# Optimization experiments

Hardware: AMD Instinct MI355X
Metric: run time of the kernel (lower is better)

Reference implementation:

```python
import jax, jax.numpy as jnp
import numpy as np

V, F, P = 1024, 2048, 8192
_EPS = 1e-12


def setup_inputs() -> dict:
    key = jax.random.key(0)
    kv, kf, kp = jax.random.split(key, 3)
    verts = jax.random.normal(kv, (V, 3), dtype=jnp.float32)
    faces = jax.random.randint(kf, (F, 3), 0, V, dtype=jnp.int32)
    points = jax.random.normal(kp, (P, 3), dtype=jnp.float32)
    return {"verts": verts, "faces": faces, "points": points}


def _closest_point_on_tri(p, a, b, c):
    """Ericson's closest-point-on-triangle, broadcast over leading dims.
    p, a, b, c: [..., 3] -> closest point [..., 3]."""
    ab = b - a
    ac = c - a
    ap = p - a
    d1 = jnp.sum(ab * ap, -1)
    d2 = jnp.sum(ac * ap, -1)
    bp = p - b
    d3 = jnp.sum(ab * bp, -1)
    d4 = jnp.sum(ac * bp, -1)
    cp = p - c
    d5 = jnp.sum(ab * cp, -1)
    d6 = jnp.sum(ac * cp, -1)
    vc = d1 * d4 - d3 * d2
    vb = d5 * d2 - d1 * d6
    va = d3 * d6 - d5 * d4
    # guarded edge/interior parameters (denominators are >0 whenever the
    # corresponding region condition holds; eps keeps unselected branches finite)
    t_ab = d1 / jnp.maximum(d1 - d3, _EPS)
    t_ac = d2 / jnp.maximum(d2 - d6, _EPS)
    t_bc = (d4 - d3) / jnp.maximum((d4 - d3) + (d5 - d6), _EPS)
    denom = jnp.maximum(va + vb + vc, _EPS)
    v_in = vb / denom
    w_in = vc / denom
    # first-match region selection (vertex A, vertex B, edge AB, vertex C, edge AC, edge BC, interior)
    cA = (d1 <= 0) & (d2 <= 0)
    cB = (d3 >= 0) & (d4 <= d3)
    cAB = (vc <= 0) & (d1 >= 0) & (d3 <= 0)
    cC = (d6 >= 0) & (d5 <= d6)
    cAC = (vb <= 0) & (d2 >= 0) & (d6 <= 0)
    cBC = (va <= 0) & ((d4 - d3) >= 0) & ((d5 - d6) >= 0)
    z = jnp.zeros_like(d1)
    o = jnp.ones_like(d1)
    bv = jnp.select([cA, cB, cAB, cC, cAC, cBC], [z, o, t_ab, z, z, 1.0 - t_bc], v_in)
    bw = jnp.select([cA, cB, cAB, cC, cAC, cBC], [z, z, z, o, t_ac, t_bc], w_in)
    bu = 1.0 - bv - bw
    return a * bu[..., None] + b * bv[..., None] + c * bw[..., None]


def reference(verts, faces, points):
    tri = verts[faces]  # [F, 3, 3]
    a = tri[:, 0][None]  # [1, F, 3]
    b = tri[:, 1][None]
    c = tri[:, 2][None]
    cp = _closest_point_on_tri(points[:, None, :], a, b, c)  # [P, F, 3]
    dist2 = jnp.sum((points[:, None, :] - cp) ** 2, -1)  # [P, F] squared distances
    assoc = jnp.argmin(dist2, axis=1).astype(jnp.int32)  # [P] nearest triangle index
    dist = jnp.min(dist2, axis=1)  # [P]
    # loss_type == 'mse': kernel loss = sum(dist), then *= 1000 / P
    loss = jnp.sum(dist) * (1000.0 / points.shape[0])
    return loss, dist, assoc
```

## Files before the change

kernel.cpp:

```cpp
#include <hip/hip_runtime.h>
#include <float.h>

#define P_TOTAL 8192
#define F_TOTAL 2048
#define TPB     256
#define CHUNK   256
#define NCHUNK  (F_TOTAL / CHUNK)

__device__ __forceinline__ float refine_rcp(float D) {
#pragma clang fp contract(off)
    float r0 = __builtin_amdgcn_rcpf(D);
    float e1 = __builtin_fmaf(-D, r0, 1.0f);
    return __builtin_fmaf(e1, r0, r0);
}
__device__ __forceinline__ float div_rn(float num, float D, float r) {
#pragma clang fp contract(off)
    float q0 = num * r;
    float e  = __builtin_fmaf(-D, q0, num);
    return __builtin_fmaf(e, r, q0);
}

__device__ __forceinline__ void region_select(
    float d1, float d2, float d3, float d4, float d5, float d6,
    float va, float vb, float vc, float d43, float d56,
    float g1, float g2, float g3, float g4,
    float& bu, float& bv, float& bw)
{
#pragma clang fp contract(off)
    float G1 = fmaxf(g1, 1e-12f);
    float G2 = fmaxf(g2, 1e-12f);
    float G3 = fmaxf(g3, 1e-12f);
    float G4 = fmaxf(g4, 1e-12f);

    bool cA  = (d1 <= 0.f) & (d2 <= 0.f);
    bool cB  = (d3 >= 0.f) & (d4 <= d3);
    bool cAB = (vc <= 0.f) & (d1 >= 0.f) & (d3 <= 0.f);
    bool cC  = (d6 >= 0.f) & (d5 <= d6);
    bool cAC = (vb <= 0.f) & (d2 >= 0.f) & (d6 <= 0.f);
    bool cBC = (va <= 0.f) & (d43 >= 0.f) & (d56 >= 0.f);

    float nv = cA ? 0.f : cB ? 1.f : cAB ? d1 : cC ? 0.f
             : cAC ? 0.f : cBC ? d43 : vb;
    float nw = cA ? 0.f : cB ? 0.f : cAB ? 0.f : cC ? 1.f
             : cAC ? d2 : cBC ? d43 : vc;
    float D  = cA ? 1.f : cB ? 1.f : cAB ? G1 : cC ? 1.f
             : cAC ? G2 : cBC ? G3 : G4;
    bool fBC = cBC && !(cA || cB || cAB || cC || cAC);

    float r   = refine_rcp(D);
    float qv  = div_rn(nv, D, r);
    float bww = div_rn(nw, D, r);
    float bvv = fBC ? (1.0f - qv) : qv;
    bv = bvv; bw = bww;
    bu = (1.0f - bvv) - bww;
}

__device__ __forceinline__ float eval_exact(
    float px, float py, float pz,
    float ax, float ay, float az,
    float bx, float by, float bz,
    float cx, float cy, float cz)
{
#pragma clang fp contract(off)
    float abx = bx - ax, aby = by - ay, abz = bz - az;
    float acx = cx - ax, acy = cy - ay, acz = cz - az;
    float apx = px - ax, apy = py - ay, apz = pz - az;
    float d1 = (abx * apx + aby * apy) + abz * apz;
    float d2 = (acx * apx + acy * apy) + acz * apz;
    float bpx = px - bx, bpy = py - by, bpz = pz - bz;
    float d3 = (abx * bpx + aby * bpy) + abz * bpz;
    float d4 = (acx * bpx + acy * bpy) + acz * bpz;
    float cpx = px - cx, cpy = py - cy, cpz = pz - cz;
    float d5 = (abx * cpx + aby * cpy) + abz * cpz;
    float d6 = (acx * cpx + acy * cpy) + acz * cpz;

    float vc = d1 * d4 - d3 * d2;
    float vb = d5 * d2 - d1 * d6;
    float va = d3 * d6 - d5 * d4;
    float d43 = d4 - d3, d56 = d5 - d6;
    float g1 = d1 - d3, g2 = d2 - d6, g3 = d43 + d56, g4 = (va + vb) + vc;

    float bu, bv, bw;
    region_select(d1, d2, d3, d4, d5, d6, va, vb, vc, d43, d56,
                  g1, g2, g3, g4, bu, bv, bw);

    float cpx2 = (ax * bu + bx * bv) + cx * bw;
    float cpy2 = (ay * bu + by * bv) + cy * bw;
    float cpz2 = (az * bu + bz * bv) + cz * bw;
    float dx = px - cpx2, dy = py - cpy2, dz = pz - cpz2;
    return (dx * dx + dy * dy) + dz * dz;
}

__global__ __launch_bounds__(TPB) void msdf_main(
    const float* __restrict__ verts, const int* __restrict__ faces,
    const float* __restrict__ points, float* __restrict__ out)
{
    __shared__ float sT[13][CHUNK];
    __shared__ int   slist[4][CHUNK];
    const int tid  = threadIdx.x;
    const int lane = tid & 63;
    const int w    = tid >> 6;
    const int p    = blockIdx.x * 4 + w;

    const float px = points[3 * p], py = points[3 * p + 1], pz = points[3 * p + 2];

    unsigned int best_bits = 0xFFFFFFFFu;
    int best_idx = 0;
    float ub = FLT_MAX;

    for (int c = 0; c < NCHUNK; ++c) {
        __syncthreads();
        {
            int tg = c * CHUNK + tid;
            int i0 = faces[3 * tg + 0], i1 = faces[3 * tg + 1], i2 = faces[3 * tg + 2];
            float ax = verts[3 * i0], ay = verts[3 * i0 + 1], az = verts[3 * i0 + 2];
            float bx = verts[3 * i1], by = verts[3 * i1 + 1], bz = verts[3 * i1 + 2];
            float cx = verts[3 * i2], cy = verts[3 * i2 + 1], cz = verts[3 * i2 + 2];
            sT[0][tid] = ax; sT[1][tid] = ay; sT[2][tid] = az;
            sT[3][tid] = bx; sT[4][tid] = by; sT[5][tid] = bz;
            sT[6][tid] = cx; sT[7][tid] = cy; sT[8][tid] = cz;
            float e1x = bx - ax, e1y = by - ay, e1z = bz - az;
            float e2x = cx - ax, e2y = cy - ay, e2z = cz - az;
            float nx = e1y * e2z - e1z * e2y;
            float ny = e1z * e2x - e1x * e2z;
            float nz = e1x * e2y - e1y * e2x;
            float nn = (nx * nx + ny * ny) + nz * nz;
            float inv = (nn > 1e-30f) ? (1.0f / sqrtf(nn)) : 0.0f;
            nx *= inv; ny *= inv; nz *= inv;
            sT[9][tid] = nx; sT[10][tid] = ny; sT[11][tid] = nz;
            sT[12][tid] = (nx * ax + ny * ay) + nz * az;
        }
        __syncthreads();

        if (c == 0) {
            float u = FLT_MAX;
            #pragma unroll
            for (int s = 0; s < 4; ++s) {
                int t = s * 64 + lane;
                float dx = px - sT[0][t], dy = py - sT[1][t], dz = pz - sT[2][t];
                u = fminf(u, (dx * dx + dy * dy) + dz * dz);
            }
            #pragma unroll
            for (int off = 32; off; off >>= 1)
                u = fminf(u, __shfl_xor(u, off, 64));
            ub = fminf(ub, u);
        }

        int cnt = 0;
        const float ubm = ub * 1.02f + 1e-18f;
        #pragma unroll
        for (int s = 0; s < 4; ++s) {
            int t = s * 64 + lane;
            float lv = ((sT[9][t] * px + sT[10][t] * py) + sT[11][t] * pz) - sT[12][t];
            float lb = lv * lv;
            bool pred = (lb <= ubm);
            unsigned long long m = __ballot(pred);
            if (pred) {
                int off = (int)__popcll(m & ((1ull << lane) - 1ull));
                slist[w][cnt + off] = t;
            }
            cnt += (int)__popcll(m);
        }
        __threadfence_block();

        float ubc = FLT_MAX;
        for (int j = lane; j < cnt; j += 64) {
            int t = slist[w][j];
            float d2v = eval_exact(px, py, pz,
                sT[0][t], sT[1][t], sT[2][t],
                sT[3][t], sT[4][t], sT[5][t],
                sT[6][t], sT[7][t], sT[8][t]);
            unsigned int bits = __float_as_uint(d2v);
            int gi = c * CHUNK + t;
            if (bits < best_bits) { best_bits = bits; best_idx = gi; }
            ubc = fminf(ubc, d2v);
        }
        #pragma unroll
        for (int off = 32; off; off >>= 1)
            ubc = fminf(ubc, __shfl_xor(ubc, off, 64));
        ub = fminf(ub, ubc);
    }

    unsigned long long key =
        ((unsigned long long)best_bits << 32) | (unsigned int)best_idx;
    #pragma unroll
    for (int off = 32; off > 0; off >>= 1) {
        unsigned int hi = (unsigned int)(key >> 32);
        unsigned int lo = (unsigned int)(key & 0xFFFFFFFFu);
        unsigned int ohi = __shfl_down(hi, off, 64);
        unsigned int olo = __shfl_down(lo, off, 64);
        unsigned long long ok = ((unsigned long long)ohi << 32) | olo;
        key = (ok < key) ? ok : key;
    }
    if (lane == 0) {
        out[1 + p]           = __uint_as_float((unsigned int)(key >> 32));
        out[1 + P_TOTAL + p] = (float)(unsigned int)(key & 0xFFFFFFFFu);
    }
}

__global__ __launch_bounds__(256) void msdf_loss(float* __restrict__ out)
{
    __shared__ float wsum[4];
    float s = 0.f;
    for (int k = 0; k < P_TOTAL / 256; ++k)
        s += out[1 + k * 256 + threadIdx.x];
    #pragma unroll
    for (int off = 32; off > 0; off >>= 1) s += __shfl_down(s, off, 64);
    int lane = threadIdx.x & 63, w = threadIdx.x >> 6;
    if (lane == 0) wsum[w] = s;
    __syncthreads();
    if (threadIdx.x == 0) {
        float tot = ((wsum[0] + wsum[1]) + wsum[2]) + wsum[3];
        out[0] = tot * (1000.0f / (float)P_TOTAL);
    }
}

extern "C" void kernel_launch(void* const* d_in, const int* in_sizes, int n_in,
                              void* d_out, int out_size, void* d_ws, size_t ws_size,
                              hipStream_t stream) {
    const float* verts  = (const float*)d_in[0];
    const int*   faces  = (const int*)d_in[1];
    const float* points = (const float*)d_in[2];
    float* out = (float*)d_out;

    msdf_main<<<dim3(P_TOTAL / 4), dim3(TPB), 0, stream>>>(verts, faces, points, out);
    msdf_loss<<<dim3(1), dim3(256), 0, stream>>>(out);
}
```

Before: 96.70 us.

## Precompute triangle data in prep kernel and batch candidate evaluation via ring buffer

Moves per-face gathering and plane-normal computation into a separate prep kernel that writes packed float4 records to workspace, so the main kernel no longer redoes this work in every block or uses shared-memory staging with block barriers. Candidates that pass the plane-distance filter are queued per wave in a 512-entry ring buffer and evaluated only in full batches of 64, which keeps lanes busy instead of leaving them idle on partial chunks. In exchange it adds a kernel launch and reads triangle data from global memory/cache rather than LDS. The bound is also tightened less often, since it is only updated after each batch.

```diff
diff --git a/kernel.cpp b/kernel.cpp
--- a/kernel.cpp
+++ b/kernel.cpp
@@ -56,12 +56,13 @@
 }
 
 __device__ __forceinline__ float eval_exact(
-    float px, float py, float pz,
-    float ax, float ay, float az,
-    float bx, float by, float bz,
-    float cx, float cy, float cz)
-{
-#pragma clang fp contract(off)
+    float px, float py, float pz, float4 q0, float4 q1, float4 q2)
+{
+#pragma clang fp contract(off)
+    float ax = q0.x, ay = q0.y, az = q0.z;
+    float bx = q0.w, by = q1.x, bz = q1.y;
+    float cx = q1.z, cy = q1.w, cz = q2.x;
+
     float abx = bx - ax, aby = by - ay, abz = bz - az;
     float acx = cx - ax, acy = cy - ay, acz = cz - az;
     float apx = px - ax, apy = py - ay, apz = pz - az;
@@ -91,12 +92,34 @@
     return (dx * dx + dy * dy) + dz * dz;
 }
 
+__global__ __launch_bounds__(256) void msdf_prep(
+    const float* __restrict__ verts, const int* __restrict__ faces,
+    float4* __restrict__ pre_n, float4* __restrict__ pre_v)
+{
+    int t = blockIdx.x * 256 + threadIdx.x;
+    int i0 = faces[3 * t + 0], i1 = faces[3 * t + 1], i2 = faces[3 * t + 2];
+    float ax = verts[3 * i0], ay = verts[3 * i0 + 1], az = verts[3 * i0 + 2];
+    float bx = verts[3 * i1], by = verts[3 * i1 + 1], bz = verts[3 * i1 + 2];
+    float cx = verts[3 * i2], cy = verts[3 * i2 + 1], cz = verts[3 * i2 + 2];
+    float e1x = bx - ax, e1y = by - ay, e1z = bz - az;
+    float e2x = cx - ax, e2y = cy - ay, e2z = cz - az;
+    float nx = e1y * e2z - e1z * e2y;
+    float ny = e1z * e2x - e1x * e2z;
+    float nz = e1x * e2y - e1y * e2x;
+    float nn = (nx * nx + ny * ny) + nz * nz;
+    float inv = (nn > 1e-30f) ? (1.0f / sqrtf(nn)) : 0.0f;
+    nx *= inv; ny *= inv; nz *= inv;
+    pre_n[t] = make_float4(nx, ny, nz, (nx * ax + ny * ay) + nz * az);
+    pre_v[3 * t + 0] = make_float4(ax, ay, az, bx);
+    pre_v[3 * t + 1] = make_float4(by, bz, cx, cy);
+    pre_v[3 * t + 2] = make_float4(cz, 0.f, 0.f, 0.f);
+}
+
 __global__ __launch_bounds__(TPB) void msdf_main(
-    const float* __restrict__ verts, const int* __restrict__ faces,
+    const float4* __restrict__ pre_n, const float4* __restrict__ pre_v,
     const float* __restrict__ points, float* __restrict__ out)
 {
-    __shared__ float sT[13][CHUNK];
-    __shared__ int   slist[4][CHUNK];
+    __shared__ int slist[4][512];
     const int tid  = threadIdx.x;
     const int lane = tid & 63;
     const int w    = tid >> 6;
@@ -104,81 +127,55 @@
 
     const float px = points[3 * p], py = points[3 * p + 1], pz = points[3 * p + 2];
 
+    float u = FLT_MAX;
+    #pragma unroll
+    for (int s = 0; s < 4; ++s) {
+        float4 q = pre_v[3 * (s * 64 + lane)];
+        float dx = px - q.x, dy = py - q.y, dz = pz - q.z;
+        u = fminf(u, (dx * dx + dy * dy) + dz * dz);
+    }
+    #pragma unroll
+    for (int off = 32; off; off >>= 1)
+        u = fminf(u, __shfl_xor(u, off, 64));
+    float ub = u;
+
     unsigned int best_bits = 0xFFFFFFFFu;
     int best_idx = 0;
-    float ub = FLT_MAX;
+    int pend = 0, h = 0;
 
     for (int c = 0; c < NCHUNK; ++c) {
-        __syncthreads();
-        {
-            int tg = c * CHUNK + tid;
-            int i0 = faces[3 * tg + 0], i1 = faces[3 * tg + 1], i2 = faces[3 * tg + 2];
-            float ax = verts[3 * i0], ay = verts[3 * i0 + 1], az = verts[3 * i0 + 2];
-            float bx = verts[3 * i1], by = verts[3 * i1 + 1], bz = verts[3 * i1 + 2];
-            float cx = verts[3 * i2], cy = verts[3 * i2 + 1], cz = verts[3 * i2 + 2];
-            sT[0][tid] = ax; sT[1][tid] = ay; sT[2][tid] = az;
-            sT[3][tid] = bx; sT[4][tid] = by; sT[5][tid] = bz;
-            sT[6][tid] = cx; sT[7][tid] = cy; sT[8][tid] = cz;
-            float e1x = bx - ax, e1y = by - ay, e1z = bz - az;
-            float e2x = cx - ax, e2y = cy - ay, e2z = cz - az;
-            float nx = e1y * e2z - e1z * e2y;
-            float ny = e1z * e2x - e1x * e2z;
-            float nz = e1x * e2y - e1y * e2x;
-            float nn = (nx * nx + ny * ny) + nz * nz;
-            float inv = (nn > 1e-30f) ? (1.0f / sqrtf(nn)) : 0.0f;
-            nx *= inv; ny *= inv; nz *= inv;
-            sT[9][tid] = nx; sT[10][tid] = ny; sT[11][tid] = nz;
-            sT[12][tid] = (nx * ax + ny * ay) + nz * az;
-        }
-        __syncthreads();
-
-        if (c == 0) {
-            float u = FLT_MAX;
-            #pragma unroll
-            for (int s = 0; s < 4; ++s) {
-                int t = s * 64 + lane;
-                float dx = px - sT[0][t], dy = py - sT[1][t], dz = pz - sT[2][t];
-                u = fminf(u, (dx * dx + dy * dy) + dz * dz);
-            }
-            #pragma unroll
-            for (int off = 32; off; off >>= 1)
-                u = fminf(u, __shfl_xor(u, off, 64));
-            ub = fminf(ub, u);
-        }
-
-        int cnt = 0;
         const float ubm = ub * 1.02f + 1e-18f;
         #pragma unroll
         for (int s = 0; s < 4; ++s) {
-            int t = s * 64 + lane;
-            float lv = ((sT[9][t] * px + sT[10][t] * py) + sT[11][t] * pz) - sT[12][t];
-            float lb = lv * lv;
-            bool pred = (lb <= ubm);
+            int t = c * CHUNK + s * 64 + lane;
+            float4 n = pre_n[t];
+            float lv = ((n.x * px + n.y * py) + n.z * pz) - n.w;
+            bool pred = (lv * lv <= ubm);
             unsigned long long m = __ballot(pred);
             if (pred) {
                 int off = (int)__popcll(m & ((1ull << lane) - 1ull));
-                slist[w][cnt + off] = t;
+                slist[w][(h + pend + off) & 511] = t;
             }
-            cnt += (int)__popcll(m);
+            pend += (int)__popcll(m);
         }
-        __threadfence_block();
-
-        float ubc = FLT_MAX;
-        for (int j = lane; j < cnt; j += 64) {
-            int t = slist[w][j];
-            float d2v = eval_exact(px, py, pz,
-                sT[0][t], sT[1][t], sT[2][t],
-                sT[3][t], sT[4][t], sT[5][t],
-                sT[6][t], sT[7][t], sT[8][t]);
+        bool drain = (c == 0) || (c == NCHUNK - 1);
+        while (pend >= 64 || (drain && pend > 0)) {
+            int n_ev = pend < 64 ? pend : 64;
+            int j = (lane < n_ev) ? lane : 0;
+            int t = slist[w][(h + j) & 511];
+            float4 q0 = pre_v[3 * t + 0];
+            float4 q1 = pre_v[3 * t + 1];
+            float4 q2 = pre_v[3 * t + 2];
+            float d2v = eval_exact(px, py, pz, q0, q1, q2);
             unsigned int bits = __float_as_uint(d2v);
-            int gi = c * CHUNK + t;
-            if (bits < best_bits) { best_bits = bits; best_idx = gi; }
-            ubc = fminf(ubc, d2v);
+            if (bits < best_bits) { best_bits = bits; best_idx = t; }
+            float ubc = d2v;
+            #pragma unroll
+            for (int off = 32; off; off >>= 1)
+                ubc = fminf(ubc, __shfl_xor(ubc, off, 64));
+            ub = fminf(ub, ubc);
+            h += n_ev; pend -= n_ev;
         }
-        #pragma unroll
-        for (int off = 32; off; off >>= 1)
-            ubc = fminf(ubc, __shfl_xor(ubc, off, 64));
-        ub = fminf(ub, ubc);
     }
 
     unsigned long long key =
@@ -222,7 +219,10 @@
     const int*   faces  = (const int*)d_in[1];
     const float* points = (const float*)d_in[2];
     float* out = (float*)d_out;
-
-    msdf_main<<<dim3(P_TOTAL / 4), dim3(TPB), 0, stream>>>(verts, faces, points, out);
+    float4* pre_n = (float4*)d_ws;
+    float4* pre_v = (float4*)((char*)d_ws + F_TOTAL * sizeof(float4));
+
+    msdf_prep<<<dim3(F_TOTAL / 256), dim3(256), 0, stream>>>(verts, faces, pre_n, pre_v);
+    msdf_main<<<dim3(P_TOTAL / 4), dim3(TPB), 0, stream>>>(pre_n, pre_v, points, out);
     msdf_loss<<<dim3(1), dim3(256), 0, stream>>>(out);
 }
```

Result: faster. 88.03 us (-9.0%).
